# Kernel tuning notes

Hardware: AMD Instinct MI355X
Metric: run time of the kernel (lower is better)

## Reference

```python
import jax, jax.numpy as jnp
import numpy as np
import math

D_MODEL = 1024
N_HEAD = 16


def setup_inputs() -> dict:
    key = jax.random.key(0)
    k1, k2, k3 = jax.random.split(key, 3)
    B, S, E = 2, 2048, D_MODEL
    x = jax.random.normal(k1, (B, S, E), dtype=jnp.float32)
    # Linear weights stored as (in, out); init scaled like typical transformer init
    w_attn = jax.random.normal(k2, (E, 3 * E), dtype=jnp.float32) * (1.0 / math.sqrt(E))
    w_proj = jax.random.normal(k3, (E, E), dtype=jnp.float32) * (1.0 / math.sqrt(E))
    return {"x": x, "w_attn": w_attn, "w_proj": w_proj}


def reference(x, w_attn, w_proj):
    B, S, E = x.shape
    H = N_HEAD
    Dh = E // H
    qkv = x @ w_attn  # (B, S, 3E)
    q, k, v = jnp.split(qkv, 3, axis=-1)
    # (B, H, S, Dh)
    q = q.reshape(B, S, H, Dh).transpose(0, 2, 1, 3)
    k = k.reshape(B, S, H, Dh).transpose(0, 2, 1, 3)
    v = v.reshape(B, S, H, Dh).transpose(0, 2, 1, 3)
    scale = 1.0 / math.sqrt(Dh)
    att = jnp.einsum('bhqd,bhkd->bhqk', q, k) * scale  # (B, H, S, S)
    causal = jnp.tril(jnp.ones((S, S), dtype=bool))
    att = jnp.where(causal, att, -jnp.inf)
    att = jax.nn.softmax(att, axis=-1)
    # dropout = 0.0 (eval mode) -> identity
    y = jnp.einsum('bhqk,bhkd->bhqd', att, v)  # (B, H, S, Dh)
    y = y.transpose(0, 2, 1, 3).reshape(B, S, E)
    return y @ w_proj
```

## Files before the change

kernel.cpp:

```cpp
#include <hip/hip_runtime.h>
#include <hip/hip_bf16.h>

#define S_LEN 2048
#define EMB   1024
#define NH    16
#define DH    64
#define QKV_LD 3072

typedef __attribute__((ext_vector_type(8)))  __bf16 bf16x8;
typedef __attribute__((ext_vector_type(4)))  __bf16 bf16x4;
typedef __attribute__((ext_vector_type(4)))  float  f32x4;
typedef __attribute__((ext_vector_type(16))) float  f32x16;
typedef __attribute__((ext_vector_type(2)))  unsigned int u32x2;

__device__ __forceinline__ void gl_lds16(const void* g, void* l) {
  __builtin_amdgcn_global_load_lds(
      (const __attribute__((address_space(1))) void*)g,
      (__attribute__((address_space(3))) void*)l,
      16, 0, 0);
}

__global__ __launch_bounds__(256)
void prep_fused(const float* __restrict__ x, __bf16* __restrict__ xb,
                const float* __restrict__ w_attn, __bf16* __restrict__ wat,
                const float* __restrict__ w_proj, __bf16* __restrict__ wpt,
                int n8) {
  __shared__ float T[64][65];
  const int bid = blockIdx.x;
  const int tid = threadIdx.x;

  if (bid < 2048) {
    int i = bid * 256 + tid;
    if (i >= n8) return;
    const f32x4* p = (const f32x4*)(x + (size_t)i * 8);
    f32x4 a = p[0], b = p[1];
    bf16x8 o;
    #pragma unroll
    for (int j = 0; j < 4; j++) { o[j] = (__bf16)a[j]; o[4 + j] = (__bf16)b[j]; }
    *(bf16x8*)(xb + (size_t)i * 8) = o;
    return;
  }

  const float* W; __bf16* Wt; int K, N, k0, n0;
  if (bid < 2048 + 768) {
    int t = bid - 2048;
    W = w_attn; Wt = wat; K = 1024; N = 3072;
    n0 = (t % 48) * 64; k0 = (t / 48) * 64;
  } else {
    int t = bid - 2816;
    W = w_proj; Wt = wpt; K = 1024; N = 1024;
    n0 = (t & 15) * 64; k0 = (t >> 4) * 64;
  }
  #pragma unroll
  for (int t = 0; t < 16; t++) {
    int idx = tid + t * 256;
    int r = idx >> 6, c = idx & 63;
    T[r][c] = W[(size_t)(k0 + r) * N + n0 + c];
  }
  __syncthreads();
  #pragma unroll
  for (int t = 0; t < 16; t++) {
    int idx = tid + t * 256;
    int r = idx >> 6, c = idx & 63;
    Wt[(size_t)(n0 + r) * K + k0 + c] = (__bf16)T[c][r];
  }
}

#define TM 128
#define TK 32

template <typename OutT, int TNv>
__global__ __launch_bounds__(256, 2)
void gemm_bf16_mfma(const __bf16* __restrict__ A, const __bf16* __restrict__ Bt,
                    OutT* __restrict__ C, int M, int N, int K) {
  __shared__ __align__(16) __bf16 As[2][TM][TK];
  __shared__ __align__(16) __bf16 Bs[2][TNv][TK];
  const int tid  = threadIdx.x;
  const int lane = tid & 63;
  const int w    = tid >> 6;
  const int wr   = w >> 1, wc = w & 1;
  const int brow = blockIdx.y * TM;
  const int bcol = blockIdx.x * TNv;
  const int l15  = lane & 15;
  const int grp  = lane >> 4;

  constexpr int NBI = TNv / 64;
  constexpr int WCT = TNv / 2;
  constexpr int NN  = WCT / 16;

  auto stage = [&](int k0, int buf) {
    #pragma unroll
    for (int j = 0; j < 2; j++) {
      const int cid = w * 128 + j * 64 + lane;
      const int row = cid >> 2, k8 = (cid & 3) * 8;
      gl_lds16(A + (size_t)(brow + row) * K + k0 + k8,
               &As[buf][0][0] + (size_t)(w * 128 + j * 64) * 8);
    }
    #pragma unroll
    for (int j = 0; j < NBI; j++) {
      const int cid = (w * NBI + j) * 64 + lane;
      const int row = cid >> 2, k8 = (cid & 3) * 8;
      gl_lds16(Bt + (size_t)(bcol + row) * K + k0 + k8,
               &Bs[buf][0][0] + (size_t)((w * NBI + j) * 64) * 8);
    }
  };

  f32x4 acc[4][NN];
  #pragma unroll
  for (int m = 0; m < 4; m++)
    #pragma unroll
    for (int n = 0; n < NN; n++) acc[m][n] = (f32x4){0.f, 0.f, 0.f, 0.f};

  stage(0, 0);
  __syncthreads();

  const int nk = K / TK;
  for (int kt = 0; kt < nk; kt++) {
    const int cur = kt & 1;
    if (kt + 1 < nk) stage((kt + 1) * TK, cur ^ 1);

    bf16x8 a[4], b[NN];
    #pragma unroll
    for (int m = 0; m < 4; m++)
      a[m] = *(const bf16x8*)&As[cur][wr * 64 + m * 16 + l15][grp * 8];
    #pragma unroll
    for (int n = 0; n < NN; n++)
      b[n] = *(const bf16x8*)&Bs[cur][wc * WCT + n * 16 + l15][grp * 8];
    #pragma unroll
    for (int m = 0; m < 4; m++)
      #pragma unroll
      for (int n = 0; n < NN; n++)
        acc[m][n] = __builtin_amdgcn_mfma_f32_16x16x32_bf16(a[m], b[n], acc[m][n], 0, 0, 0);

    __syncthreads();
  }

  #pragma unroll
  for (int m = 0; m < 4; m++)
    #pragma unroll
    for (int r = 0; r < 4; r++) {
      const size_t row = (size_t)(brow + wr * 64 + m * 16 + grp * 4 + r);
      #pragma unroll
      for (int n = 0; n < NN; n++)
        C[row * N + bcol + wc * WCT + n * 16 + l15] = (OutT)acc[m][n][r];
    }
}

#define QB 64
#define KB 64
#define QSCALE 0.18033688f

__device__ __constant__ unsigned char ITEMS[44] = {
  76, 72, 68, 64,
  125, 127, 121, 60,
  123, 117, 119, 113, 56,
  115, 109, 111, 105, 52,
  107, 101, 103, 97, 48,
  99, 93, 95, 89, 44,
  91, 85, 87, 81, 40,
  83, 36,
  32, 28, 24, 20, 16, 12, 8, 4, 0
};

__global__ __launch_bounds__(256, 4)
void attn_mfma(const __bf16* __restrict__ qkv, __bf16* __restrict__ y,
               float* __restrict__ pO, float* __restrict__ pml) {
  __shared__ __align__(16) char SMEM[17408];
  __bf16 (*Ks)[64] = (__bf16 (*)[64])SMEM;
  __bf16* Vs = (__bf16*)(SMEM + 8192);

  const int tid  = threadIdx.x;
  const int lane = tid & 63;
  const int w    = tid >> 6;

  const int bid = blockIdx.x;
  const int xcd = bid & 7;
  const int j   = bid >> 3;
  const int g   = xcd * 4 + j / 44;
  const int idx = j % 44;

  const int code  = ITEMS[idx];
  const bool split = code & 1;
  const int khalf = (code >> 1) & 1;
  const int qtile = code >> 2;

  int it0, it1;
  bool diag;
  if (!split) {
    it0 = 0; it1 = qtile + 1; diag = true;
  } else {
    const int half = (qtile + 2) >> 1;
    it0 = khalf ? half : 0;
    it1 = khalf ? qtile + 1 : half;
    diag = (khalf == 1);
  }
  const int h = g & 15, b = g >> 4;
  const int pidx = split ? ((g * 12 + (qtile - 20)) * 2 + khalf) : 0;

  const __bf16* base = qkv + (size_t)b * S_LEN * QKV_LD;

  const int l31 = lane & 31;
  const int hl  = lane >> 5;
  const int qh  = w >> 1;
  const int kh  = w & 1;

  const int voff32 = ((lane >> 4) & 1) * 2048 + hl * 128 + (lane & 15) * 8
                   + kh * 1024;

  auto stageK = [&](int j0) {
    #pragma unroll
    for (int jj = 0; jj < 2; jj++) {
      const int cid = w * 128 + jj * 64 + lane;
      const int r = cid >> 3, pc = cid & 7;
      const int lc = pc ^ (r & 7);
      gl_lds16(base + (size_t)(j0 + r) * QKV_LD + EMB + h * DH + lc * 8,
               SMEM + (w * 128 + jj * 64) * 16);
    }
  };
  auto stageV = [&](int j0) {
    #pragma unroll
    for (int jj = 0; jj < 2; jj++) {
      const int cid = w * 128 + jj * 64 + lane;
      const int db = cid >> 7, sk = (cid >> 3) & 15;
      const int jr = (cid >> 1) & 3, ch = cid & 1;
      gl_lds16(base + (size_t)(j0 + sk * 4 + jr) * QKV_LD + 2 * EMB + h * DH
                    + db * 16 + ch * 8,
               SMEM + 8192 + (w * 128 + jj * 64) * 16);
    }
  };

  const int qbase = qtile * QB;
  const int q = qbase + qh * 32 + l31;

  bf16x8 qf[4];
  {
    const __bf16* qp = base + (size_t)q * QKV_LD + h * DH;
    #pragma unroll
    for (int dq = 0; dq < 4; dq++) {
      bf16x8 v = *(const bf16x8*)(qp + dq * 16 + hl * 8);
      #pragma unroll
      for (int i2 = 0; i2 < 8; i2++) qf[dq][i2] = (__bf16)((float)v[i2] * QSCALE);
    }
  }

  f32x16 o_acc[2];
  #pragma unroll
  for (int d2 = 0; d2 < 2; d2++)
    #pragma unroll
    for (int r = 0; r < 16; r++) o_acc[d2][r] = 0.f;
  float m = -1e30f, l = 0.f;

  auto iter = [&](int j0, bool masked, int jn, bool do_stage) {
    asm volatile("s_waitcnt vmcnt(0)" ::: "memory");
    __builtin_amdgcn_s_barrier();
    __builtin_amdgcn_sched_barrier(0);

    f32x16 s;
    #pragma unroll
    for (int r = 0; r < 16; r++) s[r] = 0.f;
    const int krow = kh * 32 + l31;
    __builtin_amdgcn_s_setprio(1);
    #pragma unroll
    for (int dq = 0; dq < 4; dq++) {
      bf16x8 kf = *(const bf16x8*)&Ks[krow][((dq * 2 + hl) ^ (krow & 7)) * 8];
      s = __builtin_amdgcn_mfma_f32_32x32x16_bf16(kf, qf[dq], s, 0, 0, 0);
    }
    __builtin_amdgcn_s_setprio(0);

    if (masked) {
      const int lim = q - j0 - kh * 32 - 4 * hl;
      #pragma unroll
      for (int r = 0; r < 16; r++) {
        const int kl = (r & 3) + 8 * (r >> 2);
        if (kl > lim) s[r] = -2e30f;
      }
    }

    const unsigned vb =
        (unsigned)(uintptr_t)(__attribute__((address_space(3))) char*)(Vs)
        + (unsigned)voff32;
    u32x2 tv[8];
    asm volatile("ds_read_b64_tr_b16 %0, %1 offset:0"    : "=v"(tv[0]) : "v"(vb));
    asm volatile("ds_read_b64_tr_b16 %0, %1 offset:256"  : "=v"(tv[1]) : "v"(vb));
    asm volatile("ds_read_b64_tr_b16 %0, %1 offset:512"  : "=v"(tv[2]) : "v"(vb));
    asm volatile("ds_read_b64_tr_b16 %0, %1 offset:768"  : "=v"(tv[3]) : "v"(vb));
    asm volatile("ds_read_b64_tr_b16 %0, %1 offset:4096" : "=v"(tv[4]) : "v"(vb));
    asm volatile("ds_read_b64_tr_b16 %0, %1 offset:4352" : "=v"(tv[5]) : "v"(vb));
    asm volatile("ds_read_b64_tr_b16 %0, %1 offset:4608" : "=v"(tv[6]) : "v"(vb));
    asm volatile("ds_read_b64_tr_b16 %0, %1 offset:4864" : "=v"(tv[7]) : "v"(vb));

    float x0 = fmaxf(s[0], s[8]),  x1 = fmaxf(s[1], s[9]);
    float x2 = fmaxf(s[2], s[10]), x3 = fmaxf(s[3], s[11]);
    float x4 = fmaxf(s[4], s[12]), x5 = fmaxf(s[5], s[13]);
    float x6 = fmaxf(s[6], s[14]), x7 = fmaxf(s[7], s[15]);
    x0 = fmaxf(x0, x4); x1 = fmaxf(x1, x5);
    x2 = fmaxf(x2, x6); x3 = fmaxf(x3, x7);
    x0 = fmaxf(x0, x2); x1 = fmaxf(x1, x3);
    float tmax = fmaxf(x0, x1);
    tmax = fmaxf(tmax, __shfl_xor(tmax, 32));

    const bool grow = !__all(tmax <= m + 8.0f);
    float corr = 1.f;
    if (grow) {
      const float mnew = fmaxf(m, tmax);
      corr = __builtin_amdgcn_exp2f(m - mnew);
      m = mnew;
    }

    __builtin_amdgcn_s_barrier();
    if (do_stage) stageK(jn);

    asm volatile("s_waitcnt lgkmcnt(0)" ::: "memory");
    __builtin_amdgcn_sched_barrier(0);
    __builtin_amdgcn_s_barrier();
    if (do_stage) stageV(jn);

    float ps0 = 0.f, ps1 = 0.f, ps2 = 0.f, ps3 = 0.f;
    #pragma unroll
    for (int r = 0; r < 16; r += 4) {
      float p0 = __builtin_amdgcn_exp2f(s[r]     - m);
      float p1 = __builtin_amdgcn_exp2f(s[r + 1] - m);
      float p2 = __builtin_amdgcn_exp2f(s[r + 2] - m);
      float p3 = __builtin_amdgcn_exp2f(s[r + 3] - m);
      s[r] = p0; s[r + 1] = p1; s[r + 2] = p2; s[r + 3] = p3;
      ps0 += p0; ps1 += p1; ps2 += p2; ps3 += p3;
    }
    float psum = (ps0 + ps1) + (ps2 + ps3);

    bf16x8 pb0, pb1;
    #pragma unroll
    for (int i2 = 0; i2 < 8; i2++) {
      pb0[i2] = (__bf16)s[i2];
      pb1[i2] = (__bf16)s[8 + i2];
    }

    if (grow) {
      #pragma unroll
      for (int d2 = 0; d2 < 2; d2++)
        #pragma unroll
        for (int r = 0; r < 16; r++) o_acc[d2][r] *= corr;
    }

    __builtin_amdgcn_s_setprio(1);
    #pragma unroll
    for (int d2 = 0; d2 < 2; d2++) {
      bf16x8 a0, a1;
      ((u32x2*)&a0)[0] = tv[d2 * 4 + 0]; ((u32x2*)&a0)[1] = tv[d2 * 4 + 1];
      ((u32x2*)&a1)[0] = tv[d2 * 4 + 2]; ((u32x2*)&a1)[1] = tv[d2 * 4 + 3];
      o_acc[d2] = __builtin_amdgcn_mfma_f32_32x32x16_bf16(a0, pb0, o_acc[d2], 0, 0, 0);
      o_acc[d2] = __builtin_amdgcn_mfma_f32_32x32x16_bf16(a1, pb1, o_acc[d2], 0, 0, 0);
    }
    __builtin_amdgcn_s_setprio(0);

    psum += __shfl_xor(psum, 32);
    l = grow ? (l * corr + psum) : (l + psum);
  };

  stageK(it0 * KB);
  stageV(it0 * KB);

  const int nt = it1 - it0;
  #pragma unroll 1
  for (int tt = 0; tt < nt; tt++) {
    iter((it0 + tt) * KB, (tt == nt - 1) && diag,
         (it0 + tt + 1) * KB, tt + 1 < nt);
  }

  __syncthreads();
  float* exO  = (float*)SMEM;
  float* exML = (float*)(SMEM + 16384);
  const int slot = qh * 64 + lane;
  if (kh) {
    #pragma unroll
    for (int r = 0; r < 16; r++) {
      exO[r * 128 + slot]        = o_acc[0][r];
      exO[(16 + r) * 128 + slot] = o_acc[1][r];
    }
    exML[slot]       = m;
    exML[128 + slot] = l;
  }
  __syncthreads();
  if (!kh) {
    const float m1  = exML[slot];
    const float l1v = exML[128 + slot];
    const float mm = fmaxf(m, m1);
    const float c0 = __builtin_amdgcn_exp2f(m - mm);
    const float c1 = __builtin_amdgcn_exp2f(m1 - mm);
    const float lsum = l * c0 + l1v * c1;
    if (split) {
      float* prow = pO + (size_t)pidx * 4096 + (size_t)(qh * 32 + l31) * 64;
      #pragma unroll
      for (int d2 = 0; d2 < 2; d2++)
        #pragma unroll
        for (int rq = 0; rq < 4; rq++) {
          f32x4 o4;
          #pragma unroll
          for (int jj = 0; jj < 4; jj++) {
            const int r = rq * 4 + jj;
            o4[jj] = o_acc[d2][r] * c0 + exO[(d2 * 16 + r) * 128 + slot] * c1;
          }
          *(f32x4*)&prow[d2 * 32 + rq * 8 + hl * 4] = o4;
        }
      if (!hl) {
        pml[(size_t)pidx * 128 + qh * 32 + l31]      = mm;
        pml[(size_t)pidx * 128 + 64 + qh * 32 + l31] = lsum;
      }
    } else {
      const float inv = 1.f / lsum;
      __bf16* yrow = y + ((size_t)(b * S_LEN + q)) * EMB + h * DH;
      #pragma unroll
      for (int d2 = 0; d2 < 2; d2++)
        #pragma unroll
        for (int rq = 0; rq < 4; rq++) {
          bf16x4 o4;
          #pragma unroll
          for (int jj = 0; jj < 4; jj++) {
            const int r = rq * 4 + jj;
            float v = (o_acc[d2][r] * c0 + exO[(d2 * 16 + r) * 128 + slot] * c1) * inv;
            o4[jj] = (__bf16)v;
          }
          *(bf16x4*)&yrow[d2 * 32 + rq * 8 + hl * 4] = o4;
        }
    }
  }
}

__global__ __launch_bounds__(256)
void attn_merge(const float* __restrict__ pO, const float* __restrict__ pml,
                __bf16* __restrict__ y) {
  const int mid = blockIdx.x;
  const int g = mid / 12, qrel = mid % 12;
  const int qt = 20 + qrel;
  const int b = g >> 4, h = g & 15;
  const int p0 = (g * 12 + qrel) * 2, p1 = p0 + 1;
  const int row = threadIdx.x >> 2;
  const int d0  = (threadIdx.x & 3) * 16;

  const float mA = pml[(size_t)p0 * 128 + row];
  const float lA = pml[(size_t)p0 * 128 + 64 + row];
  const float mB = pml[(size_t)p1 * 128 + row];
  const float lB = pml[(size_t)p1 * 128 + 64 + row];
  const float mm = fmaxf(mA, mB);
  const float cA = __builtin_amdgcn_exp2f(mA - mm);
  const float cB = __builtin_amdgcn_exp2f(mB - mm);
  const float inv = 1.f / (lA * cA + lB * cB);

  const float* OA = pO + (size_t)p0 * 4096 + (size_t)row * 64 + d0;
  const float* OB = pO + (size_t)p1 * 4096 + (size_t)row * 64 + d0;
  __bf16* yr = y + ((size_t)(b * S_LEN + qt * 64 + row)) * EMB + h * DH + d0;
  #pragma unroll
  for (int i = 0; i < 4; i++) {
    f32x4 va = *(const f32x4*)(OA + i * 4);
    f32x4 vb = *(const f32x4*)(OB + i * 4);
    bf16x4 o;
    #pragma unroll
    for (int jj = 0; jj < 4; jj++)
      o[jj] = (__bf16)((va[jj] * cA + vb[jj] * cB) * inv);
    *(bf16x4*)(yr + i * 4) = o;
  }
}

extern "C" void kernel_launch(void* const* d_in, const int* in_sizes, int n_in,
                              void* d_out, int out_size, void* d_ws, size_t ws_size,
                              hipStream_t stream) {
  const float* x      = (const float*)d_in[0];
  const float* w_attn = (const float*)d_in[1];
  const float* w_proj = (const float*)d_in[2];
  float* out = (float*)d_out;

  const int B = in_sizes[0] / (S_LEN * EMB);
  const int M = B * S_LEN;

  __bf16* xb   = (__bf16*)d_ws;
  __bf16* wat  = xb  + (size_t)M * EMB;
  __bf16* wpt  = wat + (size_t)QKV_LD * EMB;
  __bf16* qkvb = wpt + (size_t)EMB * EMB;
  __bf16* yb   = qkvb + (size_t)M * QKV_LD;

  float* pO  = (float*)d_ws;
  float* pml = pO + (size_t)768 * 4096;

  {
    int n8 = (M * EMB) / 8;
    prep_fused<<<dim3(3072), 256, 0, stream>>>(x, xb, w_attn, wat, w_proj, wpt, n8);
  }

  dim3 g1(QKV_LD / 128, M / TM);
  gemm_bf16_mfma<__bf16, 128><<<g1, 256, 0, stream>>>(xb, wat, qkvb, M, QKV_LD, EMB);

  attn_mfma<<<dim3(1408), 256, 0, stream>>>(qkvb, yb, pO, pml);
  attn_merge<<<dim3(384), 256, 0, stream>>>(pO, pml, yb);

  dim3 g3(EMB / 64, M / TM);
  gemm_bf16_mfma<float, 64><<<g3, 256, 0, stream>>>(yb, wpt, out, M, EMB, EMB);
}
```

Measured before the change: 109.6 us.

## Rebalance causal attention work by pairing q-tiles into fewer equal-cost blocks

Replaces the per-block item table with a two-segment schedule in which each block may process two q-tile ranges back to back, pairing short and long causal rows so blocks have roughly equal KV iterations. The grid drops from 1408 to 992 blocks, and the split range moves to q-tiles 19-31 with a matching merge grid and partial buffer layout. The aim is to reduce tail imbalance and per-block launch overhead. The cost is a per-segment Q reload, extra barriers between segments, and a larger partial-result buffer.

```diff
diff --git a/kernel.cpp b/kernel.cpp
--- a/kernel.cpp
+++ b/kernel.cpp
@@ -150,16 +150,38 @@
 #define KB 64
 #define QSCALE 0.18033688f
 
-__device__ __constant__ unsigned char ITEMS[44] = {
-  76, 72, 68, 64,
-  125, 127, 121, 60,
-  123, 117, 119, 113, 56,
-  115, 109, 111, 105, 52,
-  107, 101, 103, 97, 48,
-  99, 93, 95, 89, 44,
-  91, 85, 87, 81, 40,
-  83, 36,
-  32, 28, 24, 20, 16, 12, 8, 4, 0
+__device__ __constant__ unsigned char ITB[31][8] = {
+  {18,0,19,2, 255,0,0,0},
+  {17,0,18,2, 255,0,0,0},
+  {19,0,17,1, 255,0,0,0},
+  {20,0,17,1, 255,0,0,0},
+  {21,0,17,1, 255,0,0,0},
+  {22,0,17,1, 255,0,0,0},
+  {23,0,17,1, 255,0,0,0},
+  {24,0,17,1, 255,0,0,0},
+  {25,0,17,1, 255,0,0,0},
+  {26,0,17,1, 255,0,0,0},
+  {27,0,17,1, 255,0,0,0},
+  {28,0,17,1, 255,0,0,0},
+  {29,0,17,1, 255,0,0,0},
+  {30,0,17,1, 255,0,0,0},
+  {31,0,17,1, 255,0,0,0},
+  {16,0,17,2, 255,0,0,0},
+  {31,17,32,3, 255,0,0,0},
+  { 0,0, 1,2,  15,0,16,2},
+  { 1,0, 2,2,  14,0,15,2},
+  { 2,0, 3,2,  13,0,14,2},
+  { 3,0, 4,2,  12,0,13,2},
+  { 4,0, 5,2,  11,0,12,2},
+  { 5,0, 6,2,  10,0,11,2},
+  { 6,0, 7,2,   9,0,10,2},
+  { 7,0, 8,2,   8,0, 9,2},
+  {19,17,20,3, 30,17,31,3},
+  {20,17,21,3, 29,17,30,3},
+  {21,17,22,3, 28,17,29,3},
+  {22,17,23,3, 27,17,28,3},
+  {23,17,24,3, 26,17,27,3},
+  {24,17,25,3, 25,17,26,3},
 };
 
 __global__ __launch_bounds__(256, 4)
@@ -173,29 +195,12 @@
   const int lane = tid & 63;
   const int w    = tid >> 6;
 
-  const int bid = blockIdx.x;
-  const int xcd = bid & 7;
-  const int j   = bid >> 3;
-  const int g   = xcd * 4 + j / 44;
-  const int idx = j % 44;
-
-  const int code  = ITEMS[idx];
-  const bool split = code & 1;
-  const int khalf = (code >> 1) & 1;
-  const int qtile = code >> 2;
-
-  int it0, it1;
-  bool diag;
-  if (!split) {
-    it0 = 0; it1 = qtile + 1; diag = true;
-  } else {
-    const int half = (qtile + 2) >> 1;
-    it0 = khalf ? half : 0;
-    it1 = khalf ? qtile + 1 : half;
-    diag = (khalf == 1);
-  }
+  const int bid  = blockIdx.x;
+  const int xcd  = bid & 7;
+  const int slot = bid >> 3;
+  const int g    = xcd * 4 + slot / 31;
+  const int idx  = slot % 31;
   const int h = g & 15, b = g >> 4;
-  const int pidx = split ? ((g * 12 + (qtile - 20)) * 2 + khalf) : 0;
 
   const __bf16* base = qkv + (size_t)b * S_LEN * QKV_LD;
 
@@ -229,26 +234,10 @@
     }
   };
 
-  const int qbase = qtile * QB;
-  const int q = qbase + qh * 32 + l31;
-
+  f32x16 o_acc[2];
+  float m, l;
+  int q;
   bf16x8 qf[4];
-  {
-    const __bf16* qp = base + (size_t)q * QKV_LD + h * DH;
-    #pragma unroll
-    for (int dq = 0; dq < 4; dq++) {
-      bf16x8 v = *(const bf16x8*)(qp + dq * 16 + hl * 8);
-      #pragma unroll
-      for (int i2 = 0; i2 < 8; i2++) qf[dq][i2] = (__bf16)((float)v[i2] * QSCALE);
-    }
-  }
-
-  f32x16 o_acc[2];
-  #pragma unroll
-  for (int d2 = 0; d2 < 2; d2++)
-    #pragma unroll
-    for (int r = 0; r < 16; r++) o_acc[d2][r] = 0.f;
-  float m = -1e30f, l = 0.f;
 
   auto iter = [&](int j0, bool masked, int jn, bool do_stage) {
     asm volatile("s_waitcnt vmcnt(0)" ::: "memory");
@@ -356,72 +345,101 @@
     l = grow ? (l * corr + psum) : (l + psum);
   };
 
-  stageK(it0 * KB);
-  stageV(it0 * KB);
-
-  const int nt = it1 - it0;
   #pragma unroll 1
-  for (int tt = 0; tt < nt; tt++) {
-    iter((it0 + tt) * KB, (tt == nt - 1) && diag,
-         (it0 + tt + 1) * KB, tt + 1 < nt);
-  }
-
-  __syncthreads();
-  float* exO  = (float*)SMEM;
-  float* exML = (float*)(SMEM + 16384);
-  const int slot = qh * 64 + lane;
-  if (kh) {
-    #pragma unroll
-    for (int r = 0; r < 16; r++) {
-      exO[r * 128 + slot]        = o_acc[0][r];
-      exO[(16 + r) * 128 + slot] = o_acc[1][r];
-    }
-    exML[slot]       = m;
-    exML[128 + slot] = l;
-  }
-  __syncthreads();
-  if (!kh) {
-    const float m1  = exML[slot];
-    const float l1v = exML[128 + slot];
-    const float mm = fmaxf(m, m1);
-    const float c0 = __builtin_amdgcn_exp2f(m - mm);
-    const float c1 = __builtin_amdgcn_exp2f(m1 - mm);
-    const float lsum = l * c0 + l1v * c1;
-    if (split) {
-      float* prow = pO + (size_t)pidx * 4096 + (size_t)(qh * 32 + l31) * 64;
-      #pragma unroll
-      for (int d2 = 0; d2 < 2; d2++)
+  for (int seg = 0; seg < 2; seg++) {
+    const int qtile = ITB[idx][seg * 4 + 0];
+    if (qtile == 255) break;
+    const int it0 = ITB[idx][seg * 4 + 1];
+    const int it1 = ITB[idx][seg * 4 + 2];
+    const int fl  = ITB[idx][seg * 4 + 3];
+    const bool split = fl & 1;
+    const bool diag  = (fl >> 1) & 1;
+
+    q = qtile * QB + qh * 32 + l31;
+    {
+      const __bf16* qp = base + (size_t)q * QKV_LD + h * DH;
+      #pragma unroll
+      for (int dq = 0; dq < 4; dq++) {
+        bf16x8 v = *(const bf16x8*)(qp + dq * 16 + hl * 8);
         #pragma unroll
-        for (int rq = 0; rq < 4; rq++) {
-          f32x4 o4;
+        for (int i2 = 0; i2 < 8; i2++) qf[dq][i2] = (__bf16)((float)v[i2] * QSCALE);
+      }
+    }
+    #pragma unroll
+    for (int d2 = 0; d2 < 2; d2++)
+      #pragma unroll
+      for (int r = 0; r < 16; r++) o_acc[d2][r] = 0.f;
+    m = -1e30f; l = 0.f;
+
+    stageK(it0 * KB);
+    stageV(it0 * KB);
+
+    const int nt = it1 - it0;
+    #pragma unroll 1
+    for (int tt = 0; tt < nt; tt++) {
+      iter((it0 + tt) * KB, (tt == nt - 1) && diag,
+           (it0 + tt + 1) * KB, tt + 1 < nt);
+    }
+
+    __syncthreads();
+    float* exO  = (float*)SMEM;
+    float* exML = (float*)(SMEM + 16384);
+    const int slot2 = qh * 64 + lane;
+    if (kh) {
+      #pragma unroll
+      for (int r = 0; r < 16; r++) {
+        exO[r * 128 + slot2]        = o_acc[0][r];
+        exO[(16 + r) * 128 + slot2] = o_acc[1][r];
+      }
+      exML[slot2]       = m;
+      exML[128 + slot2] = l;
+    }
+    __syncthreads();
+    if (!kh) {
+      const float m1  = exML[slot2];
+      const float l1v = exML[128 + slot2];
+      const float mm = fmaxf(m, m1);
+      const float c0 = __builtin_amdgcn_exp2f(m - mm);
+      const float c1 = __builtin_amdgcn_exp2f(m1 - mm);
+      const float lsum = l * c0 + l1v * c1;
+      if (split) {
+        const int pidx = (g * 13 + (qtile - 19)) * 2 + (it0 ? 1 : 0);
+        float* prow = pO + (size_t)pidx * 4096 + (size_t)(qh * 32 + l31) * 64;
+        #pragma unroll
+        for (int d2 = 0; d2 < 2; d2++)
           #pragma unroll
-          for (int jj = 0; jj < 4; jj++) {
-            const int r = rq * 4 + jj;
-            o4[jj] = o_acc[d2][r] * c0 + exO[(d2 * 16 + r) * 128 + slot] * c1;
+          for (int rq = 0; rq < 4; rq++) {
+            f32x4 o4;
+            #pragma unroll
+            for (int jj = 0; jj < 4; jj++) {
+              const int r = rq * 4 + jj;
+              o4[jj] = o_acc[d2][r] * c0 + exO[(d2 * 16 + r) * 128 + slot2] * c1;
+            }
+            *(f32x4*)&prow[d2 * 32 + rq * 8 + hl * 4] = o4;
           }
-          *(f32x4*)&prow[d2 * 32 + rq * 8 + hl * 4] = o4;
+        if (!hl) {
+          pml[(size_t)pidx * 128 + qh * 32 + l31]      = mm;
+          pml[(size_t)pidx * 128 + 64 + qh * 32 + l31] = lsum;
         }
-      if (!hl) {
-        pml[(size_t)pidx * 128 + qh * 32 + l31]      = mm;
-        pml[(size_t)pidx * 128 + 64 + qh * 32 + l31] = lsum;
+      } else {
+        const float inv = 1.f / lsum;
+        __bf16* yrow = y + ((size_t)(b * S_LEN + q)) * EMB + h * DH;
+        #pragma unroll
+        for (int d2 = 0; d2 < 2; d2++)
+          #pragma unroll
+          for (int rq = 0; rq < 4; rq++) {
+            bf16x4 o4;
+            #pragma unroll
+            for (int jj = 0; jj < 4; jj++) {
+              const int r = rq * 4 + jj;
+              float v = (o_acc[d2][r] * c0 + exO[(d2 * 16 + r) * 128 + slot2] * c1) * inv;
+              o4[jj] = (__bf16)v;
+            }
+            *(bf16x4*)&yrow[d2 * 32 + rq * 8 + hl * 4] = o4;
+          }
       }
-    } else {
-      const float inv = 1.f / lsum;
-      __bf16* yrow = y + ((size_t)(b * S_LEN + q)) * EMB + h * DH;
-      #pragma unroll
-      for (int d2 = 0; d2 < 2; d2++)
-        #pragma unroll
-        for (int rq = 0; rq < 4; rq++) {
-          bf16x4 o4;
-          #pragma unroll
-          for (int jj = 0; jj < 4; jj++) {
-            const int r = rq * 4 + jj;
-            float v = (o_acc[d2][r] * c0 + exO[(d2 * 16 + r) * 128 + slot] * c1) * inv;
-            o4[jj] = (__bf16)v;
-          }
-          *(bf16x4*)&yrow[d2 * 32 + rq * 8 + hl * 4] = o4;
-        }
-    }
+    }
+    __syncthreads();
   }
 }
 
@@ -429,10 +447,10 @@
 void attn_merge(const float* __restrict__ pO, const float* __restrict__ pml,
                 __bf16* __restrict__ y) {
   const int mid = blockIdx.x;
-  const int g = mid / 12, qrel = mid % 12;
-  const int qt = 20 + qrel;
+  const int g = mid / 13, qrel = mid % 13;
+  const int qt = 19 + qrel;
   const int b = g >> 4, h = g & 15;
-  const int p0 = (g * 12 + qrel) * 2, p1 = p0 + 1;
+  const int p0 = (g * 13 + qrel) * 2, p1 = p0 + 1;
   const int row = threadIdx.x >> 2;
   const int d0  = (threadIdx.x & 3) * 16;
 
@@ -478,7 +496,7 @@
   __bf16* yb   = qkvb + (size_t)M * QKV_LD;
 
   float* pO  = (float*)d_ws;
-  float* pml = pO + (size_t)768 * 4096;
+  float* pml = pO + (size_t)832 * 4096;
 
   {
     int n8 = (M * EMB) / 8;
@@ -488,8 +506,8 @@
   dim3 g1(QKV_LD / 128, M / TM);
   gemm_bf16_mfma<__bf16, 128><<<g1, 256, 0, stream>>>(xb, wat, qkvb, M, QKV_LD, EMB);
 
-  attn_mfma<<<dim3(1408), 256, 0, stream>>>(qkvb, yb, pO, pml);
-  attn_merge<<<dim3(384), 256, 0, stream>>>(pO, pml, yb);
+  attn_mfma<<<dim3(992), 256, 0, stream>>>(qkvb, yb, pO, pml);
+  attn_merge<<<dim3(416), 256, 0, stream>>>(pO, pml, yb);
 
   dim3 g3(EMB / 64, M / TM);
   gemm_bf16_mfma<float, 64><<<g3, 256, 0, stream>>>(yb, wpt, out, M, EMB, EMB);
```

Result: slower. 115.8 us (+5.6%).
